# Performance work log

Hardware: AMD Instinct MI355X
Metric: run time of the kernel (lower is better)

Reference implementation:

```python
import jax, jax.numpy as jnp
import numpy as np

D_MODEL = 1024
NUM_HEADS = 16
DEPTH = D_MODEL // NUM_HEADS


def setup_inputs() -> dict:
    key = jax.random.key(0)
    ks = jax.random.split(key, 12)
    B, S = 2, 2048
    s = 1.0 / np.sqrt(D_MODEL)
    return {
        "q": jax.random.normal(ks[0], (B, S, D_MODEL), jnp.float32),
        "k": jax.random.normal(ks[1], (B, S, D_MODEL), jnp.float32),
        "v": jax.random.normal(ks[2], (B, S, D_MODEL), jnp.float32),
        "wq": jax.random.normal(ks[3], (D_MODEL, D_MODEL), jnp.float32) * s,
        "bq": jnp.zeros((D_MODEL,), jnp.float32),
        "wk": jax.random.normal(ks[4], (D_MODEL, D_MODEL), jnp.float32) * s,
        "bk": jnp.zeros((D_MODEL,), jnp.float32),
        "wv": jax.random.normal(ks[5], (D_MODEL, D_MODEL), jnp.float32) * s,
        "bv": jnp.zeros((D_MODEL,), jnp.float32),
        "wo": jax.random.normal(ks[6], (D_MODEL, D_MODEL), jnp.float32) * s,
        "bo": jnp.zeros((D_MODEL,), jnp.float32),
    }


def _split_heads(x):
    B, S, _ = x.shape
    return x.reshape(B, S, NUM_HEADS, DEPTH).transpose(0, 2, 1, 3)  # [B,H,S,d]


def reference(q, k, v, wq, bq, wk, bk, wv, bv, wo, bo):
    B, S, _ = q.shape
    qh = _split_heads(q @ wq + bq)
    kh = _split_heads(k @ wk + bk)
    vh = _split_heads(v @ wv + bv)
    scale = 1.0 / jnp.sqrt(jnp.asarray(DEPTH, jnp.float32))
    logits = jnp.einsum("bhqd,bhkd->bhqk", qh, kh) * scale  # [B,H,S,S]
    attn = jax.nn.softmax(logits, axis=-1)
    ctx = jnp.einsum("bhqk,bhkd->bhqd", attn, vh)
    ctx = ctx.transpose(0, 2, 1, 3).reshape(B, S, D_MODEL)
    out = ctx @ wo + bo
    return out, attn
```

## Files before the change

### kernel.cpp

```cpp
#include <hip/hip_runtime.h>
#include <math.h>

#define D_MODEL   1024
#define NUM_HEADS 16
#define DEPTH     64
#define S_LEN     2048
#define BATCH     2

typedef __attribute__((ext_vector_type(4))) float  f32x4;
typedef __attribute__((ext_vector_type(8))) __bf16 bf16x8;
typedef __attribute__((ext_vector_type(4))) __bf16 bf16x4;

__device__ __forceinline__ void split2(float x, __bf16& h, __bf16& l) {
    h = (__bf16)x;
    l = (__bf16)(x - (float)h);
}

__device__ __forceinline__ int frag2(int r, int k) {
    return (((r >> 4) * 2 + (k >> 5)) << 10) + (((k >> 3) & 3) << 8) + ((r & 15) << 4);
}
__device__ __forceinline__ int frag4(int r, int k) {
    return (((r >> 4) * 4 + (k >> 5)) << 10) + (((k >> 3) & 3) << 8) + ((r & 15) << 4);
}

__device__ __forceinline__ f32x4 mm16(bf16x8 a, bf16x8 b, f32x4 c) {
    return __builtin_amdgcn_mfma_f32_16x16x32_bf16(a, b, c, 0, 0, 0);
}

__device__ __forceinline__ void split8(f32x4 x0, f32x4 x1, bf16x8& vh, bf16x8& vl) {
#pragma unroll
    for (int j = 0; j < 4; ++j) {
        __bf16 h, l;
        split2(x0[j], h, l); vh[j] = h;     vl[j] = l;
        split2(x1[j], h, l); vh[j + 4] = h; vl[j + 4] = l;
    }
}

__global__ __launch_bounds__(256) void wsplit(const float* __restrict__ w0,
                                              const float* __restrict__ w1,
                                              const float* __restrict__ w2,
                                              const float* __restrict__ w3,
                                              __bf16* __restrict__ base)
{
    const int z = blockIdx.z;
    const float* W = (z == 0) ? w0 : (z == 1) ? w1 : (z == 2) ? w2 : w3;
    const size_t hi_off = (z == 3) ? 0 : (size_t)(z + 1) * 2097152;
    __bf16* Hi = base + hi_off;
    __bf16* Lo = Hi + 1048576;

    __shared__ float T[64][65];
    const int tid = threadIdx.x;
    const int k0 = blockIdx.x * 64, n0 = blockIdx.y * 64;
    const int rr = tid / 16, cc = (tid % 16) * 4;

#pragma unroll
    for (int p = 0; p < 4; ++p) {
        int r = p * 16 + rr;
        f32x4 v = *(const f32x4*)&W[(size_t)(k0 + r) * 1024 + n0 + cc];
        T[r][cc + 0] = v[0]; T[r][cc + 1] = v[1];
        T[r][cc + 2] = v[2]; T[r][cc + 3] = v[3];
    }
    __syncthreads();
#pragma unroll
    for (int p = 0; p < 4; ++p) {
        int nr = p * 16 + rr;
        bf16x4 vh, vl;
#pragma unroll
        for (int j = 0; j < 4; ++j) {
            __bf16 h, l;
            split2(T[cc + j][nr], h, l);
            vh[j] = h; vl[j] = l;
        }
        *(bf16x4*)&Hi[(size_t)(n0 + nr) * 1024 + k0 + cc] = vh;
        *(bf16x4*)&Lo[(size_t)(n0 + nr) * 1024 + k0 + cc] = vl;
    }
}

__global__ __launch_bounds__(512) void gemm_split(
    const float* __restrict__ A,
    const __bf16* __restrict__ BtHi, const __bf16* __restrict__ BtLo,
    const float* __restrict__ bias,
    __bf16* __restrict__ oHi, __bf16* __restrict__ oLo,
    float* __restrict__ oF, int mode)
{
    __shared__ __align__(16) char lds[65536];
    char* AH = lds;
    char* AL = lds + 16384;
    char* BH = lds + 32768;
    char* BL = lds + 49152;

    const int tid = threadIdx.x;
    const int lane = tid & 63, wid = tid >> 6;
    const int wm = wid >> 2, wn = wid & 3;
    const int bm = blockIdx.x * 128, bn = blockIdx.y * 128;

    const int r0 = tid >> 3, kc8 = (tid & 7) * 8;
    const int r1 = r0 + 64;
    const size_t a0 = (size_t)(bm + r0) * 1024 + kc8;
    const size_t a1 = (size_t)(bm + r1) * 1024 + kc8;
    const size_t b0 = (size_t)(bn + r0) * 1024 + kc8;
    const size_t b1 = (size_t)(bn + r1) * 1024 + kc8;
    const int la0 = frag2(r0, kc8), la1 = frag2(r1, kc8);

    const f32x4 zero = {0.f, 0.f, 0.f, 0.f};
    f32x4 acc[4][2];
#pragma unroll
    for (int i = 0; i < 4; ++i) { acc[i][0] = zero; acc[i][1] = zero; }

    f32x4 x0 = *(const f32x4*)(A + a0), x1 = *(const f32x4*)(A + a0 + 4);
    f32x4 x2 = *(const f32x4*)(A + a1), x3 = *(const f32x4*)(A + a1 + 4);
    bf16x8 bh0 = *(const bf16x8*)(BtHi + b0);
    bf16x8 bh1 = *(const bf16x8*)(BtHi + b1);
    bf16x8 bl0 = *(const bf16x8*)(BtLo + b0);
    bf16x8 bl1 = *(const bf16x8*)(BtLo + b1);

    for (int k0 = 0; k0 < 1024; k0 += 64) {
        bf16x8 ah0, al0, ah1, al1;
        split8(x0, x1, ah0, al0);
        split8(x2, x3, ah1, al1);
        __syncthreads();
        *(bf16x8*)(AH + la0) = ah0; *(bf16x8*)(AL + la0) = al0;
        *(bf16x8*)(AH + la1) = ah1; *(bf16x8*)(AL + la1) = al1;
        *(bf16x8*)(BH + la0) = bh0; *(bf16x8*)(BH + la1) = bh1;
        *(bf16x8*)(BL + la0) = bl0; *(bf16x8*)(BL + la1) = bl1;
        __syncthreads();
        if (k0 + 64 < 1024) {
            const int kn = k0 + 64;
            x0 = *(const f32x4*)(A + a0 + kn); x1 = *(const f32x4*)(A + a0 + kn + 4);
            x2 = *(const f32x4*)(A + a1 + kn); x3 = *(const f32x4*)(A + a1 + kn + 4);
            bh0 = *(const bf16x8*)(BtHi + b0 + kn);
            bh1 = *(const bf16x8*)(BtHi + b1 + kn);
            bl0 = *(const bf16x8*)(BtLo + b0 + kn);
            bl1 = *(const bf16x8*)(BtLo + b1 + kn);
        }
#pragma unroll
        for (int kf = 0; kf < 2; ++kf) {
            bf16x8 fah[4], fal[4], fbh[2], fbl[2];
#pragma unroll
            for (int mf = 0; mf < 4; ++mf) {
                const int off = (((wm * 4 + mf) * 2 + kf) << 10) + lane * 16;
                fah[mf] = *(const bf16x8*)(AH + off);
                fal[mf] = *(const bf16x8*)(AL + off);
            }
#pragma unroll
            for (int nf = 0; nf < 2; ++nf) {
                const int off = (((wn * 2 + nf) * 2 + kf) << 10) + lane * 16;
                fbh[nf] = *(const bf16x8*)(BH + off);
                fbl[nf] = *(const bf16x8*)(BL + off);
            }
#pragma unroll
            for (int mf = 0; mf < 4; ++mf)
#pragma unroll
                for (int nf = 0; nf < 2; ++nf) {
                    acc[mf][nf] = mm16(fal[mf], fbh[nf], acc[mf][nf]);
                    acc[mf][nf] = mm16(fah[mf], fbl[nf], acc[mf][nf]);
                    acc[mf][nf] = mm16(fah[mf], fbh[nf], acc[mf][nf]);
                }
        }
    }

    const int rbase = (lane >> 4) * 4;
    const int cloc = lane & 15;
#pragma unroll
    for (int mf = 0; mf < 4; ++mf) {
        const int m0g = bm + wm * 64 + mf * 16 + rbase;
#pragma unroll
        for (int nf = 0; nf < 2; ++nf) {
            const int n_g = bn + wn * 32 + nf * 16 + cloc;
            const float bv = bias[n_g];
            float v[4];
#pragma unroll
            for (int r = 0; r < 4; ++r) {
                v[r] = acc[mf][nf][r] + bv;
                if (mode == 3) v[r] *= 0.125f;
            }
            if (mode == 1) {
#pragma unroll
                for (int r = 0; r < 4; ++r) oF[(size_t)(m0g + r) * 1024 + n_g] = v[r];
            } else {
                const int bb = m0g >> 11;
                const int sloc = m0g & 2047;
                const int h = n_g >> 6, d = n_g & 63;
                if (mode != 2) {
                    const size_t i0 = ((size_t)(bb * 16 + h) * 2048 + sloc) * 64 + d;
#pragma unroll
                    for (int r = 0; r < 4; ++r) {
                        __bf16 hh, ll;
                        split2(v[r], hh, ll);
                        oHi[i0 + (size_t)r * 64] = hh;
                        oLo[i0 + (size_t)r * 64] = ll;
                    }
                } else {
                    const size_t i0 = ((size_t)(bb * 16 + h) * 64 + d) * 2048 + sloc;
                    bf16x4 vh, vl;
#pragma unroll
                    for (int r = 0; r < 4; ++r) {
                        __bf16 hh, ll;
                        split2(v[r], hh, ll);
                        vh[r] = hh; vl[r] = ll;
                    }
                    *(bf16x4*)&oHi[i0] = vh;
                    *(bf16x4*)&oLo[i0] = vl;
                }
            }
        }
    }
}

__global__ __launch_bounds__(512) void attn_fused(
    const __bf16* __restrict__ QHi, const __bf16* __restrict__ QLo,
    const __bf16* __restrict__ KHi, const __bf16* __restrict__ KLo,
    const __bf16* __restrict__ VtHi, const __bf16* __restrict__ VtLo,
    float* __restrict__ attn, float* __restrict__ ctxb)
{
    __shared__ __align__(16) char lds[65536];
    char* KV = lds;
    char* PB = lds + 32768;
    float* scr = (float*)PB;

    const int tid = threadIdx.x;
    const int lane = tid & 63, wid = tid >> 6;
    const int wm = wid >> 2, wn = wid & 3;

    const int id = blockIdx.x;
    const int bh = (id & 7) + (id >> 7) * 8;
    const int bm = ((id >> 3) & 15) * 128;

    const __bf16* Qh_ = QHi + (size_t)bh * S_LEN * 64;
    const __bf16* Ql_ = QLo + (size_t)bh * S_LEN * 64;
    const __bf16* Kh_ = KHi + (size_t)bh * S_LEN * 64;
    const __bf16* Kl_ = KLo + (size_t)bh * S_LEN * 64;
    const __bf16* Vh_ = VtHi + (size_t)bh * 64 * S_LEN;
    const __bf16* Vl_ = VtLo + (size_t)bh * 64 * S_LEN;
    float* attn_b = attn + (size_t)bh * S_LEN * S_LEN;

    bf16x8 qh[4][2], ql[4][2];
#pragma unroll
    for (int mf = 0; mf < 4; ++mf)
#pragma unroll
        for (int kf = 0; kf < 2; ++kf) {
            const int row = bm + wm * 64 + mf * 16 + (lane & 15);
            const int k = kf * 32 + (lane >> 4) * 8;
            qh[mf][kf] = *(const bf16x8*)(Qh_ + (size_t)row * 64 + k);
            ql[mf][kf] = *(const bf16x8*)(Ql_ + (size_t)row * 64 + k);
        }

    const int r0 = tid >> 3, kc8 = (tid & 7) * 8;
    const int lk0 = frag2(r0, kc8), lk1 = frag2(r0 + 64, kc8);
    const int lv0 = frag4(r0, kc8), lv1 = frag4(r0, kc8 + 64);

    auto qk_tile = [&](f32x4 (&acc)[4][2]) {
        const f32x4 z4 = {0.f, 0.f, 0.f, 0.f};
#pragma unroll
        for (int i = 0; i < 4; ++i) { acc[i][0] = z4; acc[i][1] = z4; }
#pragma unroll
        for (int kf = 0; kf < 2; ++kf) {
            bf16x8 kbh[2], kbl[2];
#pragma unroll
            for (int nf = 0; nf < 2; ++nf) {
                const int off = (((wn * 2 + nf) * 2 + kf) << 10) + lane * 16;
                kbh[nf] = *(const bf16x8*)(KV + off);
                kbl[nf] = *(const bf16x8*)(KV + 16384 + off);
            }
#pragma unroll
            for (int mf = 0; mf < 4; ++mf)
#pragma unroll
                for (int nf = 0; nf < 2; ++nf) {
                    acc[mf][nf] = mm16(ql[mf][kf], kbh[nf], acc[mf][nf]);
                    acc[mf][nf] = mm16(qh[mf][kf], kbl[nf], acc[mf][nf]);
                    acc[mf][nf] = mm16(qh[mf][kf], kbh[nf], acc[mf][nf]);
                }
        }
    };

    float m_r[4][4], l_r[4][4];
#pragma unroll
    for (int mf = 0; mf < 4; ++mf)
#pragma unroll
        for (int r = 0; r < 4; ++r) { m_r[mf][r] = -INFINITY; l_r[mf][r] = 0.f; }

    bf16x8 pkh0 = *(const bf16x8*)(Kh_ + (size_t)r0 * 64 + kc8);
    bf16x8 pkh1 = *(const bf16x8*)(Kh_ + (size_t)(r0 + 64) * 64 + kc8);
    bf16x8 pkl0 = *(const bf16x8*)(Kl_ + (size_t)r0 * 64 + kc8);
    bf16x8 pkl1 = *(const bf16x8*)(Kl_ + (size_t)(r0 + 64) * 64 + kc8);

    for (int t = 0; t < 16; ++t) {
        __syncthreads();
        *(bf16x8*)(KV + lk0) = pkh0; *(bf16x8*)(KV + lk1) = pkh1;
        *(bf16x8*)(KV + 16384 + lk0) = pkl0; *(bf16x8*)(KV + 16384 + lk1) = pkl1;
        __syncthreads();
        if (t < 15) {
            const size_t g = (size_t)((t + 1) * 128) * 64 + kc8;
            pkh0 = *(const bf16x8*)(Kh_ + g + (size_t)r0 * 64);
            pkh1 = *(const bf16x8*)(Kh_ + g + (size_t)(r0 + 64) * 64);
            pkl0 = *(const bf16x8*)(Kl_ + g + (size_t)r0 * 64);
            pkl1 = *(const bf16x8*)(Kl_ + g + (size_t)(r0 + 64) * 64);
        }
        f32x4 acc[4][2];
        qk_tile(acc);
#pragma unroll
        for (int mf = 0; mf < 4; ++mf)
#pragma unroll
            for (int r = 0; r < 4; ++r) {
                const float s0 = acc[mf][0][r], s1 = acc[mf][1][r];
                const float mo = m_r[mf][r];
                const float mn = fmaxf(mo, fmaxf(s0, s1));
                l_r[mf][r] = l_r[mf][r] * __expf(mo - mn) + __expf(s0 - mn) + __expf(s1 - mn);
                m_r[mf][r] = mn;
            }
    }

#pragma unroll
    for (int mf = 0; mf < 4; ++mf)
#pragma unroll
        for (int r = 0; r < 4; ++r) {
            float m = m_r[mf][r], l = l_r[mf][r];
#pragma unroll
            for (int mask = 1; mask < 16; mask <<= 1) {
                const float m2 = __shfl_xor(m, mask);
                const float l2 = __shfl_xor(l, mask);
                const float mm = fmaxf(m, m2);
                l = l * __expf(m - mm) + l2 * __expf(m2 - mm);
                m = mm;
            }
            m_r[mf][r] = m; l_r[mf][r] = l;
        }
    if ((lane & 15) == 0) {
#pragma unroll
        for (int mf = 0; mf < 4; ++mf)
#pragma unroll
            for (int r = 0; r < 4; ++r) {
                const int row = wm * 64 + mf * 16 + (lane >> 4) * 4 + r;
                scr[(wn * 128 + row) * 2 + 0] = m_r[mf][r];
                scr[(wn * 128 + row) * 2 + 1] = l_r[mf][r];
            }
    }
    __syncthreads();
#pragma unroll
    for (int mf = 0; mf < 4; ++mf)
#pragma unroll
        for (int r = 0; r < 4; ++r) {
            const int row = wm * 64 + mf * 16 + (lane >> 4) * 4 + r;
            float m = scr[row * 2 + 0], l = scr[row * 2 + 1];
#pragma unroll
            for (int w2 = 1; w2 < 4; ++w2) {
                const float m2 = scr[(w2 * 128 + row) * 2 + 0];
                const float l2 = scr[(w2 * 128 + row) * 2 + 1];
                const float mm = fmaxf(m, m2);
                l = l * __expf(m - mm) + l2 * __expf(m2 - mm);
                m = mm;
            }
            m_r[mf][r] = m;
            l_r[mf][r] = 1.0f / l;
        }
    __syncthreads();

    const f32x4 zero = {0.f, 0.f, 0.f, 0.f};
    f32x4 pv[4];
#pragma unroll
    for (int i = 0; i < 4; ++i) pv[i] = zero;

    pkh0 = *(const bf16x8*)(Kh_ + (size_t)r0 * 64 + kc8);
    pkh1 = *(const bf16x8*)(Kh_ + (size_t)(r0 + 64) * 64 + kc8);
    pkl0 = *(const bf16x8*)(Kl_ + (size_t)r0 * 64 + kc8);
    pkl1 = *(const bf16x8*)(Kl_ + (size_t)(r0 + 64) * 64 + kc8);

    for (int t = 0; t < 16; ++t) {
        __syncthreads();
        *(bf16x8*)(KV + lk0) = pkh0; *(bf16x8*)(KV + lk1) = pkh1;
        *(bf16x8*)(KV + 16384 + lk0) = pkl0; *(bf16x8*)(KV + 16384 + lk1) = pkl1;
        __syncthreads();
        bf16x8 vh0, vh1, vl0, vl1;
        {
            const size_t gv = (size_t)r0 * S_LEN + t * 128;
            vh0 = *(const bf16x8*)(Vh_ + gv + kc8);
            vh1 = *(const bf16x8*)(Vh_ + gv + kc8 + 64);
            vl0 = *(const bf16x8*)(Vl_ + gv + kc8);
            vl1 = *(const bf16x8*)(Vl_ + gv + kc8 + 64);
        }
        if (t < 15) {
            const size_t g = (size_t)((t + 1) * 128) * 64 + kc8;
            pkh0 = *(const bf16x8*)(Kh_ + g + (size_t)r0 * 64);
            pkh1 = *(const bf16x8*)(Kh_ + g + (size_t)(r0 + 64) * 64);
            pkl0 = *(const bf16x8*)(Kl_ + g + (size_t)r0 * 64);
            pkl1 = *(const bf16x8*)(Kl_ + g + (size_t)(r0 + 64) * 64);
        }
        f32x4 acc[4][2];
        qk_tile(acc);
#pragma unroll
        for (int mf = 0; mf < 4; ++mf) {
            const int rg0 = bm + wm * 64 + mf * 16 + (lane >> 4) * 4;
#pragma unroll
            for (int nf = 0; nf < 2; ++nf) {
                const int col = t * 128 + wn * 32 + nf * 16 + (lane & 15);
#pragma unroll
                for (int r = 0; r < 4; ++r) {
                    const float p = __expf(acc[mf][nf][r] - m_r[mf][r]) * l_r[mf][r];
                    acc[mf][nf][r] = p;
                    attn_b[(size_t)(rg0 + r) * S_LEN + col] = p;
                }
            }
        }
        __syncthreads();
        *(bf16x8*)(KV + lv0) = vh0; *(bf16x8*)(KV + lv1) = vh1;
        *(bf16x8*)(KV + 16384 + lv0) = vl0; *(bf16x8*)(KV + 16384 + lv1) = vl1;
        if (wn < 2) {
#pragma unroll
            for (int mf = 0; mf < 4; ++mf)
#pragma unroll
                for (int nf = 0; nf < 2; ++nf) {
                    const int k = (wn & 1) * 32 + nf * 16 + (lane & 15);
#pragma unroll
                    for (int r = 0; r < 4; ++r) {
                        const int rl = wm * 64 + mf * 16 + (lane >> 4) * 4 + r;
                        const int off = (((rl >> 4) * 2 + (k >> 5)) << 10) +
                                        (((k >> 3) & 3) << 8) + ((rl & 15) << 4) + ((k & 7) << 1);
                        __bf16 h, l;
                        split2(acc[mf][nf][r], h, l);
                        *(__bf16*)(PB + off) = h;
                        *(__bf16*)(PB + 16384 + off) = l;
                    }
                }
        }
        __syncthreads();
#pragma unroll
        for (int kf = 0; kf < 2; ++kf) {
            const int offv = ((wn * 4 + 0 + kf) << 10) + lane * 16;
            const bf16x8 vhf = *(const bf16x8*)(KV + offv);
            const bf16x8 vlf = *(const bf16x8*)(KV + 16384 + offv);
#pragma unroll
            for (int mf = 0; mf < 4; ++mf) {
                const int offp = (((wm * 4 + mf) * 2 + kf) << 10) + lane * 16;
                const bf16x8 ph = *(const bf16x8*)(PB + offp);
                const bf16x8 pl = *(const bf16x8*)(PB + 16384 + offp);
                pv[mf] = mm16(pl, vhf, pv[mf]);
                pv[mf] = mm16(ph, vlf, pv[mf]);
                pv[mf] = mm16(ph, vhf, pv[mf]);
            }
        }
        __syncthreads();
        if (wn >= 2) {
#pragma unroll
            for (int mf = 0; mf < 4; ++mf)
#pragma unroll
                for (int nf = 0; nf < 2; ++nf) {
                    const int k = (wn & 1) * 32 + nf * 16 + (lane & 15);
#pragma unroll
                    for (int r = 0; r < 4; ++r) {
                        const int rl = wm * 64 + mf * 16 + (lane >> 4) * 4 + r;
                        const int off = (((rl >> 4) * 2 + (k >> 5)) << 10) +
                                        (((k >> 3) & 3) << 8) + ((rl & 15) << 4) + ((k & 7) << 1);
                        __bf16 h, l;
                        split2(acc[mf][nf][r], h, l);
                        *(__bf16*)(PB + off) = h;
                        *(__bf16*)(PB + 16384 + off) = l;
                    }
                }
        }
        __syncthreads();
#pragma unroll
        for (int kf = 0; kf < 2; ++kf) {
            const int offv = ((wn * 4 + 2 + kf) << 10) + lane * 16;
            const bf16x8 vhf = *(const bf16x8*)(KV + offv);
            const bf16x8 vlf = *(const bf16x8*)(KV + 16384 + offv);
#pragma unroll
            for (int mf = 0; mf < 4; ++mf) {
                const int offp = (((wm * 4 + mf) * 2 + kf) << 10) + lane * 16;
                const bf16x8 ph = *(const bf16x8*)(PB + offp);
                const bf16x8 pl = *(const bf16x8*)(PB + 16384 + offp);
                pv[mf] = mm16(pl, vhf, pv[mf]);
                pv[mf] = mm16(ph, vlf, pv[mf]);
                pv[mf] = mm16(ph, vhf, pv[mf]);
            }
        }
    }

#pragma unroll
    for (int mf = 0; mf < 4; ++mf)
#pragma unroll
        for (int r = 0; r < 4; ++r) {
            const int sg = bm + wm * 64 + mf * 16 + (lane >> 4) * 4 + r;
            const int d = wn * 16 + (lane & 15);
            ctxb[(size_t)sg * 1024 + bh * 64 + d] = pv[mf][r];
        }
}

extern "C" void kernel_launch(void* const* d_in, const int* in_sizes, int n_in,
                              void* d_out, int out_size, void* d_ws, size_t ws_size,
                              hipStream_t stream)
{
    const float* q  = (const float*)d_in[0];
    const float* k  = (const float*)d_in[1];
    const float* v  = (const float*)d_in[2];
    const float* wq = (const float*)d_in[3];
    const float* bq = (const float*)d_in[4];
    const float* wk = (const float*)d_in[5];
    const float* bk = (const float*)d_in[6];
    const float* wv = (const float*)d_in[7];
    const float* bv = (const float*)d_in[8];
    const float* wo = (const float*)d_in[9];
    const float* bo = (const float*)d_in[10];

    float* out  = (float*)d_out;
    float* attn = out + (size_t)BATCH * S_LEN * D_MODEL;

    char* ws = (char*)d_ws;
    const size_t MB = 1024 * 1024;
    __bf16* WB   = (__bf16*)ws;
    __bf16* QHI  = (__bf16*)(ws + 16 * MB);
    __bf16* QLO  = (__bf16*)(ws + 24 * MB);
    __bf16* KHI  = (__bf16*)(ws + 32 * MB);
    __bf16* KLO  = (__bf16*)(ws + 40 * MB);
    __bf16* VTHI = (__bf16*)(ws + 48 * MB);
    __bf16* VTLO = (__bf16*)(ws + 56 * MB);
    float*  ctxb = (float*)(ws + 4 * MB);

    const size_t W1M = 1048576;
    __bf16* WOT_HI = WB;                  __bf16* WOT_LO = WB + W1M;
    __bf16* WQT_HI = WB + 2 * W1M;        __bf16* WQT_LO = WB + 3 * W1M;
    __bf16* WKT_HI = WB + 4 * W1M;        __bf16* WKT_LO = WB + 5 * W1M;
    __bf16* WVT_HI = WB + 6 * W1M;        __bf16* WVT_LO = WB + 7 * W1M;

    wsplit<<<dim3(16, 16, 4), dim3(256), 0, stream>>>(wq, wk, wv, wo, WB);

    gemm_split<<<dim3(32, 8), dim3(512), 0, stream>>>(q, WQT_HI, WQT_LO, bq, QHI, QLO, nullptr, 3);
    gemm_split<<<dim3(32, 8), dim3(512), 0, stream>>>(k, WKT_HI, WKT_LO, bk, KHI, KLO, nullptr, 0);
    gemm_split<<<dim3(32, 8), dim3(512), 0, stream>>>(v, WVT_HI, WVT_LO, bv, VTHI, VTLO, nullptr, 2);

    const size_t HOFF = (size_t)NUM_HEADS * S_LEN * DEPTH;
    for (int b = 0; b < BATCH; ++b) {
        attn_fused<<<dim3(256), dim3(512), 0, stream>>>(
            QHI + b * HOFF, QLO + b * HOFF, KHI + b * HOFF, KLO + b * HOFF,
            VTHI + b * HOFF, VTLO + b * HOFF,
            attn + (size_t)b * NUM_HEADS * S_LEN * S_LEN, ctxb);
        gemm_split<<<dim3(16, 8), dim3(512), 0, stream>>>(
            ctxb, WOT_HI, WOT_LO, bo, nullptr, nullptr,
            out + (size_t)b * S_LEN * D_MODEL, 1);
    }
}
```

Baseline: 1.086 ms.

## Merge QKV and batch launches, use exp2 softmax with lazy max rescaling

The three projection GEMMs become one launch indexed by blockIdx.z. The two per-batch attention launches become a single launch, and the output projection runs as one launch over both batches. Q is pre-scaled by log2(e)/sqrt(d), so softmax can use a hardware exp2. The first-pass softmax skips updating the running max and rescaling when all new scores stay within 8 of the current max. Syncthreads is replaced by a custom LDS-wait plus barrier. The catch is that out_proj reads the context from the output buffer and writes to a temporary, which then needs an extra device-to-device copy of the output.

```diff
diff --git a/kernel.cpp b/kernel.cpp
--- a/kernel.cpp
+++ b/kernel.cpp
@@ -10,6 +10,18 @@
 typedef __attribute__((ext_vector_type(4))) float  f32x4;
 typedef __attribute__((ext_vector_type(8))) __bf16 bf16x8;
 typedef __attribute__((ext_vector_type(4))) __bf16 bf16x4;
+
+#if __has_builtin(__builtin_amdgcn_exp2f)
+#define E2(x) __builtin_amdgcn_exp2f(x)
+#else
+#define E2(x) exp2f(x)
+#endif
+
+__device__ __forceinline__ void bar() {
+    asm volatile("s_waitcnt lgkmcnt(0)" ::: "memory");
+    __builtin_amdgcn_s_barrier();
+    __builtin_amdgcn_sched_barrier(0);
+}
 
 __device__ __forceinline__ void split2(float x, __bf16& h, __bf16& l) {
     h = (__bf16)x;
@@ -76,13 +88,23 @@
     }
 }
 
-__global__ __launch_bounds__(512) void gemm_split(
-    const float* __restrict__ A,
-    const __bf16* __restrict__ BtHi, const __bf16* __restrict__ BtLo,
-    const float* __restrict__ bias,
-    __bf16* __restrict__ oHi, __bf16* __restrict__ oLo,
-    float* __restrict__ oF, int mode)
+__global__ __launch_bounds__(512) void qkv_proj(
+    const float* __restrict__ qi, const float* __restrict__ ki, const float* __restrict__ vi,
+    const __bf16* __restrict__ WB,
+    const float* __restrict__ bq, const float* __restrict__ bk, const float* __restrict__ bv,
+    __bf16* __restrict__ QHI, __bf16* __restrict__ QLO,
+    __bf16* __restrict__ KHI, __bf16* __restrict__ KLO,
+    __bf16* __restrict__ VTHI, __bf16* __restrict__ VTLO)
 {
+    const int z = blockIdx.z;
+    const float* A = (z == 0) ? qi : (z == 1) ? ki : vi;
+    const __bf16* BtHi = WB + (size_t)(2 + 2 * z) * 1048576;
+    const __bf16* BtLo = BtHi + 1048576;
+    const float* bias = (z == 0) ? bq : (z == 1) ? bk : bv;
+    __bf16* oHi = (z == 0) ? QHI : (z == 1) ? KHI : VTHI;
+    __bf16* oLo = (z == 0) ? QLO : (z == 1) ? KLO : VTLO;
+    const float scale = (z == 0) ? 0.18033688f : 1.0f;
+
     __shared__ __align__(16) char lds[65536];
     char* AH = lds;
     char* AL = lds + 16384;
@@ -118,12 +140,12 @@
         bf16x8 ah0, al0, ah1, al1;
         split8(x0, x1, ah0, al0);
         split8(x2, x3, ah1, al1);
-        __syncthreads();
+        bar();
         *(bf16x8*)(AH + la0) = ah0; *(bf16x8*)(AL + la0) = al0;
         *(bf16x8*)(AH + la1) = ah1; *(bf16x8*)(AL + la1) = al1;
         *(bf16x8*)(BH + la0) = bh0; *(bf16x8*)(BH + la1) = bh1;
         *(bf16x8*)(BL + la0) = bl0; *(bf16x8*)(BL + la1) = bl1;
-        __syncthreads();
+        bar();
         if (k0 + 64 < 1024) {
             const int kn = k0 + 64;
             x0 = *(const f32x4*)(A + a0 + kn); x1 = *(const f32x4*)(A + a0 + kn + 4);
@@ -167,42 +189,131 @@
 #pragma unroll
         for (int nf = 0; nf < 2; ++nf) {
             const int n_g = bn + wn * 32 + nf * 16 + cloc;
-            const float bv = bias[n_g];
+            const float bv2 = bias[n_g];
             float v[4];
 #pragma unroll
-            for (int r = 0; r < 4; ++r) {
-                v[r] = acc[mf][nf][r] + bv;
-                if (mode == 3) v[r] *= 0.125f;
-            }
-            if (mode == 1) {
-#pragma unroll
-                for (int r = 0; r < 4; ++r) oF[(size_t)(m0g + r) * 1024 + n_g] = v[r];
+            for (int r = 0; r < 4; ++r) v[r] = (acc[mf][nf][r] + bv2) * scale;
+            const int bb = m0g >> 11;
+            const int sloc = m0g & 2047;
+            const int h = n_g >> 6, d = n_g & 63;
+            if (z != 2) {
+                const size_t i0 = ((size_t)(bb * 16 + h) * 2048 + sloc) * 64 + d;
+#pragma unroll
+                for (int r = 0; r < 4; ++r) {
+                    __bf16 hh, ll;
+                    split2(v[r], hh, ll);
+                    oHi[i0 + (size_t)r * 64] = hh;
+                    oLo[i0 + (size_t)r * 64] = ll;
+                }
             } else {
-                const int bb = m0g >> 11;
-                const int sloc = m0g & 2047;
-                const int h = n_g >> 6, d = n_g & 63;
-                if (mode != 2) {
-                    const size_t i0 = ((size_t)(bb * 16 + h) * 2048 + sloc) * 64 + d;
-#pragma unroll
-                    for (int r = 0; r < 4; ++r) {
-                        __bf16 hh, ll;
-                        split2(v[r], hh, ll);
-                        oHi[i0 + (size_t)r * 64] = hh;
-                        oLo[i0 + (size_t)r * 64] = ll;
-                    }
-                } else {
-                    const size_t i0 = ((size_t)(bb * 16 + h) * 64 + d) * 2048 + sloc;
-                    bf16x4 vh, vl;
-#pragma unroll
-                    for (int r = 0; r < 4; ++r) {
-                        __bf16 hh, ll;
-                        split2(v[r], hh, ll);
-                        vh[r] = hh; vl[r] = ll;
-                    }
-                    *(bf16x4*)&oHi[i0] = vh;
-                    *(bf16x4*)&oLo[i0] = vl;
-                }
-            }
+                const size_t i0 = ((size_t)(bb * 16 + h) * 64 + d) * 2048 + sloc;
+                bf16x4 vh, vl;
+#pragma unroll
+                for (int r = 0; r < 4; ++r) {
+                    __bf16 hh, ll;
+                    split2(v[r], hh, ll);
+                    vh[r] = hh; vl[r] = ll;
+                }
+                *(bf16x4*)&oHi[i0] = vh;
+                *(bf16x4*)&oLo[i0] = vl;
+            }
+        }
+    }
+}
+
+__global__ __launch_bounds__(512) void out_proj(
+    const float* __restrict__ A,
+    const __bf16* __restrict__ BtHi, const __bf16* __restrict__ BtLo,
+    const float* __restrict__ bias, float* __restrict__ oF)
+{
+    __shared__ __align__(16) char lds[65536];
+    char* AH = lds;
+    char* AL = lds + 16384;
+    char* BH = lds + 32768;
+    char* BL = lds + 49152;
+
+    const int tid = threadIdx.x;
+    const int lane = tid & 63, wid = tid >> 6;
+    const int wm = wid >> 2, wn = wid & 3;
+    const int bm = blockIdx.x * 128, bn = blockIdx.y * 128;
+
+    const int r0 = tid >> 3, kc8 = (tid & 7) * 8;
+    const int r1 = r0 + 64;
+    const size_t a0 = (size_t)(bm + r0) * 1024 + kc8;
+    const size_t a1 = (size_t)(bm + r1) * 1024 + kc8;
+    const size_t b0 = (size_t)(bn + r0) * 1024 + kc8;
+    const size_t b1 = (size_t)(bn + r1) * 1024 + kc8;
+    const int la0 = frag2(r0, kc8), la1 = frag2(r1, kc8);
+
+    const f32x4 zero = {0.f, 0.f, 0.f, 0.f};
+    f32x4 acc[4][2];
+#pragma unroll
+    for (int i = 0; i < 4; ++i) { acc[i][0] = zero; acc[i][1] = zero; }
+
+    f32x4 x0 = *(const f32x4*)(A + a0), x1 = *(const f32x4*)(A + a0 + 4);
+    f32x4 x2 = *(const f32x4*)(A + a1), x3 = *(const f32x4*)(A + a1 + 4);
+    bf16x8 bh0 = *(const bf16x8*)(BtHi + b0);
+    bf16x8 bh1 = *(const bf16x8*)(BtHi + b1);
+    bf16x8 bl0 = *(const bf16x8*)(BtLo + b0);
+    bf16x8 bl1 = *(const bf16x8*)(BtLo + b1);
+
+    for (int k0 = 0; k0 < 1024; k0 += 64) {
+        bf16x8 ah0, al0, ah1, al1;
+        split8(x0, x1, ah0, al0);
+        split8(x2, x3, ah1, al1);
+        bar();
+        *(bf16x8*)(AH + la0) = ah0; *(bf16x8*)(AL + la0) = al0;
+        *(bf16x8*)(AH + la1) = ah1; *(bf16x8*)(AL + la1) = al1;
+        *(bf16x8*)(BH + la0) = bh0; *(bf16x8*)(BH + la1) = bh1;
+        *(bf16x8*)(BL + la0) = bl0; *(bf16x8*)(BL + la1) = bl1;
+        bar();
+        if (k0 + 64 < 1024) {
+            const int kn = k0 + 64;
+            x0 = *(const f32x4*)(A + a0 + kn); x1 = *(const f32x4*)(A + a0 + kn + 4);
+            x2 = *(const f32x4*)(A + a1 + kn); x3 = *(const f32x4*)(A + a1 + kn + 4);
+            bh0 = *(const bf16x8*)(BtHi + b0 + kn);
+            bh1 = *(const bf16x8*)(BtHi + b1 + kn);
+            bl0 = *(const bf16x8*)(BtLo + b0 + kn);
+            bl1 = *(const bf16x8*)(BtLo + b1 + kn);
+        }
+#pragma unroll
+        for (int kf = 0; kf < 2; ++kf) {
+            bf16x8 fah[4], fal[4], fbh[2], fbl[2];
+#pragma unroll
+            for (int mf = 0; mf < 4; ++mf) {
+                const int off = (((wm * 4 + mf) * 2 + kf) << 10) + lane * 16;
+                fah[mf] = *(const bf16x8*)(AH + off);
+                fal[mf] = *(const bf16x8*)(AL + off);
+            }
+#pragma unroll
+            for (int nf = 0; nf < 2; ++nf) {
+                const int off = (((wn * 2 + nf) * 2 + kf) << 10) + lane * 16;
+                fbh[nf] = *(const bf16x8*)(BH + off);
+                fbl[nf] = *(const bf16x8*)(BL + off);
+            }
+#pragma unroll
+            for (int mf = 0; mf < 4; ++mf)
+#pragma unroll
+                for (int nf = 0; nf < 2; ++nf) {
+                    acc[mf][nf] = mm16(fal[mf], fbh[nf], acc[mf][nf]);
+                    acc[mf][nf] = mm16(fah[mf], fbl[nf], acc[mf][nf]);
+                    acc[mf][nf] = mm16(fah[mf], fbh[nf], acc[mf][nf]);
+                }
+        }
+    }
+
+    const int rbase = (lane >> 4) * 4;
+    const int cloc = lane & 15;
+#pragma unroll
+    for (int mf = 0; mf < 4; ++mf) {
+        const int m0g = bm + wm * 64 + mf * 16 + rbase;
+#pragma unroll
+        for (int nf = 0; nf < 2; ++nf) {
+            const int n_g = bn + wn * 32 + nf * 16 + cloc;
+            const float bv2 = bias[n_g];
+#pragma unroll
+            for (int r = 0; r < 4; ++r)
+                oF[(size_t)(m0g + r) * 1024 + n_g] = acc[mf][nf][r] + bv2;
         }
     }
 }
@@ -211,7 +322,7 @@
     const __bf16* __restrict__ QHi, const __bf16* __restrict__ QLo,
     const __bf16* __restrict__ KHi, const __bf16* __restrict__ KLo,
     const __bf16* __restrict__ VtHi, const __bf16* __restrict__ VtLo,
-    float* __restrict__ attn, float* __restrict__ ctxb)
+    float* __restrict__ attn, float* __restrict__ ctx)
 {
     __shared__ __align__(16) char lds[65536];
     char* KV = lds;
@@ -223,7 +334,7 @@
     const int wm = wid >> 2, wn = wid & 3;
 
     const int id = blockIdx.x;
-    const int bh = (id & 7) + (id >> 7) * 8;
+    const int bh = (id & 7) * 4 + (id >> 7);
     const int bm = ((id >> 3) & 15) * 128;
 
     const __bf16* Qh_ = QHi + (size_t)bh * S_LEN * 64;
@@ -285,10 +396,10 @@
     bf16x8 pkl1 = *(const bf16x8*)(Kl_ + (size_t)(r0 + 64) * 64 + kc8);
 
     for (int t = 0; t < 16; ++t) {
-        __syncthreads();
+        bar();
         *(bf16x8*)(KV + lk0) = pkh0; *(bf16x8*)(KV + lk1) = pkh1;
         *(bf16x8*)(KV + 16384 + lk0) = pkl0; *(bf16x8*)(KV + 16384 + lk1) = pkl1;
-        __syncthreads();
+        bar();
         if (t < 15) {
             const size_t g = (size_t)((t + 1) * 128) * 64 + kc8;
             pkh0 = *(const bf16x8*)(Kh_ + g + (size_t)r0 * 64);
@@ -298,16 +409,31 @@
         }
         f32x4 acc[4][2];
         qk_tile(acc);
+        int ok = 1;
 #pragma unroll
         for (int mf = 0; mf < 4; ++mf)
 #pragma unroll
-            for (int r = 0; r < 4; ++r) {
-                const float s0 = acc[mf][0][r], s1 = acc[mf][1][r];
-                const float mo = m_r[mf][r];
-                const float mn = fmaxf(mo, fmaxf(s0, s1));
-                l_r[mf][r] = l_r[mf][r] * __expf(mo - mn) + __expf(s0 - mn) + __expf(s1 - mn);
-                m_r[mf][r] = mn;
-            }
+            for (int r = 0; r < 4; ++r)
+                ok &= (fmaxf(acc[mf][0][r], acc[mf][1][r]) <= m_r[mf][r] + 8.0f);
+        if (__all(ok)) {
+#pragma unroll
+            for (int mf = 0; mf < 4; ++mf)
+#pragma unroll
+                for (int r = 0; r < 4; ++r)
+                    l_r[mf][r] += E2(acc[mf][0][r] - m_r[mf][r]) +
+                                  E2(acc[mf][1][r] - m_r[mf][r]);
+        } else {
+#pragma unroll
+            for (int mf = 0; mf < 4; ++mf)
+#pragma unroll
+                for (int r = 0; r < 4; ++r) {
+                    const float s0 = acc[mf][0][r], s1 = acc[mf][1][r];
+                    const float mo = m_r[mf][r];
+                    const float mn = fmaxf(mo, fmaxf(s0, s1));
+                    l_r[mf][r] = l_r[mf][r] * E2(mo - mn) + E2(s0 - mn) + E2(s1 - mn);
+                    m_r[mf][r] = mn;
+                }
+        }
     }
 
 #pragma unroll
@@ -320,7 +446,7 @@
                 const float m2 = __shfl_xor(m, mask);
                 const float l2 = __shfl_xor(l, mask);
                 const float mm = fmaxf(m, m2);
-                l = l * __expf(m - mm) + l2 * __expf(m2 - mm);
+                l = l * E2(m - mm) + l2 * E2(m2 - mm);
                 m = mm;
             }
             m_r[mf][r] = m; l_r[mf][r] = l;
@@ -335,7 +461,7 @@
                 scr[(wn * 128 + row) * 2 + 1] = l_r[mf][r];
             }
     }
-    __syncthreads();
+    bar();
 #pragma unroll
     for (int mf = 0; mf < 4; ++mf)
 #pragma unroll
@@ -347,13 +473,13 @@
                 const float m2 = scr[(w2 * 128 + row) * 2 + 0];
                 const float l2 = scr[(w2 * 128 + row) * 2 + 1];
                 const float mm = fmaxf(m, m2);
-                l = l * __expf(m - mm) + l2 * __expf(m2 - mm);
+                l = l * E2(m - mm) + l2 * E2(m2 - mm);
                 m = mm;
             }
             m_r[mf][r] = m;
             l_r[mf][r] = 1.0f / l;
         }
-    __syncthreads();
+    bar();
 
     const f32x4 zero = {0.f, 0.f, 0.f, 0.f};
     f32x4 pv[4];
@@ -366,10 +492,10 @@
     pkl1 = *(const bf16x8*)(Kl_ + (size_t)(r0 + 64) * 64 + kc8);
 
     for (int t = 0; t < 16; ++t) {
-        __syncthreads();
+        bar();
         *(bf16x8*)(KV + lk0) = pkh0; *(bf16x8*)(KV + lk1) = pkh1;
         *(bf16x8*)(KV + 16384 + lk0) = pkl0; *(bf16x8*)(KV + 16384 + lk1) = pkl1;
-        __syncthreads();
+        bar();
         bf16x8 vh0, vh1, vl0, vl1;
         {
             const size_t gv = (size_t)r0 * S_LEN + t * 128;
@@ -395,13 +521,13 @@
                 const int col = t * 128 + wn * 32 + nf * 16 + (lane & 15);
 #pragma unroll
                 for (int r = 0; r < 4; ++r) {
-                    const float p = __expf(acc[mf][nf][r] - m_r[mf][r]) * l_r[mf][r];
+                    const float p = E2(acc[mf][nf][r] - m_r[mf][r]) * l_r[mf][r];
                     acc[mf][nf][r] = p;
                     attn_b[(size_t)(rg0 + r) * S_LEN + col] = p;
                 }
             }
         }
-        __syncthreads();
+        bar();
         *(bf16x8*)(KV + lv0) = vh0; *(bf16x8*)(KV + lv1) = vh1;
         *(bf16x8*)(KV + 16384 + lv0) = vl0; *(bf16x8*)(KV + 16384 + lv1) = vl1;
         if (wn < 2) {
@@ -422,7 +548,7 @@
                     }
                 }
         }
-        __syncthreads();
+        bar();
 #pragma unroll
         for (int kf = 0; kf < 2; ++kf) {
             const int offv = ((wn * 4 + 0 + kf) << 10) + lane * 16;
@@ -438,7 +564,7 @@
                 pv[mf] = mm16(ph, vhf, pv[mf]);
             }
         }
-        __syncthreads();
+        bar();
         if (wn >= 2) {
 #pragma unroll
             for (int mf = 0; mf < 4; ++mf)
@@ -457,7 +583,7 @@
                     }
                 }
         }
-        __syncthreads();
+        bar();
 #pragma unroll
         for (int kf = 0; kf < 2; ++kf) {
             const int offv = ((wn * 4 + 2 + kf) << 10) + lane * 16;
@@ -475,13 +601,14 @@
         }
     }
 
+    const int b = bh >> 4, h = bh & 15;
 #pragma unroll
     for (int mf = 0; mf < 4; ++mf)
 #pragma unroll
         for (int r = 0; r < 4; ++r) {
             const int sg = bm + wm * 64 + mf * 16 + (lane >> 4) * 4 + r;
             const int d = wn * 16 + (lane & 15);
-            ctxb[(size_t)sg * 1024 + bh * 64 + d] = pv[mf][r];
+            ctx[((size_t)b * S_LEN + sg) * D_MODEL + h * 64 + d] = pv[mf][r];
         }
 }
 
@@ -513,28 +640,21 @@
     __bf16* KLO  = (__bf16*)(ws + 40 * MB);
     __bf16* VTHI = (__bf16*)(ws + 48 * MB);
     __bf16* VTLO = (__bf16*)(ws + 56 * MB);
-    float*  ctxb = (float*)(ws + 4 * MB);
+    float*  tmp  = (float*)(ws + 16 * MB);
 
     const size_t W1M = 1048576;
-    __bf16* WOT_HI = WB;                  __bf16* WOT_LO = WB + W1M;
-    __bf16* WQT_HI = WB + 2 * W1M;        __bf16* WQT_LO = WB + 3 * W1M;
-    __bf16* WKT_HI = WB + 4 * W1M;        __bf16* WKT_LO = WB + 5 * W1M;
-    __bf16* WVT_HI = WB + 6 * W1M;        __bf16* WVT_LO = WB + 7 * W1M;
+    __bf16* WOT_HI = WB;
+    __bf16* WOT_LO = WB + W1M;
 
     wsplit<<<dim3(16, 16, 4), dim3(256), 0, stream>>>(wq, wk, wv, wo, WB);
 
-    gemm_split<<<dim3(32, 8), dim3(512), 0, stream>>>(q, WQT_HI, WQT_LO, bq, QHI, QLO, nullptr, 3);
-    gemm_split<<<dim3(32, 8), dim3(512), 0, stream>>>(k, WKT_HI, WKT_LO, bk, KHI, KLO, nullptr, 0);
-    gemm_split<<<dim3(32, 8), dim3(512), 0, stream>>>(v, WVT_HI, WVT_LO, bv, VTHI, VTLO, nullptr, 2);
-
-    const size_t HOFF = (size_t)NUM_HEADS * S_LEN * DEPTH;
-    for (int b = 0; b < BATCH; ++b) {
-        attn_fused<<<dim3(256), dim3(512), 0, stream>>>(
-            QHI + b * HOFF, QLO + b * HOFF, KHI + b * HOFF, KLO + b * HOFF,
-            VTHI + b * HOFF, VTLO + b * HOFF,
-            attn + (size_t)b * NUM_HEADS * S_LEN * S_LEN, ctxb);
-        gemm_split<<<dim3(16, 8), dim3(512), 0, stream>>>(
-            ctxb, WOT_HI, WOT_LO, bo, nullptr, nullptr,
-            out + (size_t)b * S_LEN * D_MODEL, 1);
-    }
-}
+    qkv_proj<<<dim3(32, 8, 3), dim3(512), 0, stream>>>(
+        q, k, v, WB, bq, bk, bv, QHI, QLO, KHI, KLO, VTHI, VTLO);
+
+    attn_fused<<<dim3(512), dim3(512), 0, stream>>>(
+        QHI, QLO, KHI, KLO, VTHI, VTLO, attn, out);
+
+    out_proj<<<dim3(32, 8), dim3(512), 0, stream>>>(out, WOT_HI, WOT_LO, bo, tmp);
+    hipMemcpyAsync(out, tmp, (size_t)BATCH * S_LEN * D_MODEL * sizeof(float),
+                   hipMemcpyDeviceToDevice, stream);
+}
```

After: 1.048 ms. -3.5%, faster.
